# Optimization experiments

Hardware: AMD Instinct MI355X
Metric: run time of the kernel (lower is better)

Reference implementation:

```python
import jax, jax.numpy as jnp
import numpy as np

D_MODEL = 96
D_STATE = 16
D_CONV = 3
EXPAND = 2
D_INNER = D_MODEL * EXPAND          # 192
DT_RANK = max(1, D_MODEL // 16)     # 6
N_DIRS = 4
LN_EPS = 1e-5


def setup_inputs() -> dict:
    key = jax.random.key(0)
    ks = jax.random.split(key, 10)
    B, H, W = 2, 64, 64
    x = jax.random.normal(ks[0], (B, D_MODEL, H, W), dtype=jnp.float32)
    in_proj_w = jax.random.normal(ks[1], (2 * D_INNER, D_MODEL), dtype=jnp.float32) * 0.02
    conv_w = jax.random.normal(ks[2], (D_INNER, 1, D_CONV, D_CONV), dtype=jnp.float32) * 0.1
    conv_b = jnp.zeros((D_INNER,), dtype=jnp.float32)
    proj_dim = DT_RANK + 2 * D_STATE
    x_proj_weight = jax.random.normal(ks[3], (N_DIRS, D_INNER, proj_dim), dtype=jnp.float32) * 0.02
    dt_proj_weight = jax.random.normal(ks[4], (N_DIRS, D_INNER, DT_RANK), dtype=jnp.float32) * 0.02
    dt_proj_bias = jax.random.uniform(ks[5], (N_DIRS, D_INNER), dtype=jnp.float32) * 0.1
    A_log = jnp.log(jnp.broadcast_to(jnp.arange(1, D_STATE + 1, dtype=jnp.float32), (D_INNER, D_STATE)))
    D_skip = jnp.ones((D_INNER,), dtype=jnp.float32)
    ln_gamma = jnp.ones((D_INNER,), dtype=jnp.float32)
    ln_beta = jnp.zeros((D_INNER,), dtype=jnp.float32)
    out_proj_w = jax.random.normal(ks[6], (D_MODEL, D_INNER), dtype=jnp.float32) * 0.02
    return {
        "x": x, "in_proj_w": in_proj_w, "conv_w": conv_w, "conv_b": conv_b,
        "x_proj_weight": x_proj_weight, "dt_proj_weight": dt_proj_weight,
        "dt_proj_bias": dt_proj_bias, "A_log": A_log, "D_skip": D_skip,
        "ln_gamma": ln_gamma, "ln_beta": ln_beta, "out_proj_w": out_proj_w,
    }


def _ss2d_forward(x, in_proj_w, conv_w, conv_b, x_proj_weight, dt_proj_weight,
                  dt_proj_bias, A_log, D_skip, ln_gamma, ln_beta, out_proj_w):
    B, D, H, W = x.shape
    E, N, R = D_INNER, D_STATE, DT_RANK
    L = H * W
    # in_proj
    x_flat = x.reshape(B, D, L).transpose(0, 2, 1)              # b l d
    xz = x_flat @ in_proj_w.T                                    # b l 2e
    xb, z = xz[..., :E], xz[..., E:]
    # depthwise conv + SiLU
    xb = xb.transpose(0, 2, 1).reshape(B, E, H, W)
    xb = jax.lax.conv_general_dilated(
        xb, conv_w, window_strides=(1, 1), padding="SAME",
        feature_group_count=E, dimension_numbers=("NCHW", "OIHW", "NCHW"))
    xb = xb + conv_b[None, :, None, None]
    xb = jax.nn.silu(xb)
    # 4-directional cross-scan sequences
    x_rm = xb.reshape(B, E, L)
    x_cm = xb.transpose(0, 1, 3, 2).reshape(B, E, L)
    xs = jnp.stack([x_rm, x_rm[..., ::-1], x_cm, x_cm[..., ::-1]], axis=0)  # k b e l
    # per-direction projections
    x_for = xs.transpose(0, 1, 3, 2)                             # k b l e
    x_dbl = jnp.einsum("kble,ker->kblr", x_for, x_proj_weight)
    dt_low, Bs, Cs = x_dbl[..., :R], x_dbl[..., R:R + N], x_dbl[..., R + N:]
    dts = jnp.einsum("kblr,ker->kble", dt_low, dt_proj_weight) + dt_proj_bias[:, None, None, :]
    dt = jax.nn.softplus(dts)                                    # k b l e
    A = -jnp.exp(A_log)                                          # e n
    # batched selective scan over (k*b)
    KB = N_DIRS * B
    u = xs.reshape(KB, E, L)
    dt_ = dt.transpose(0, 1, 3, 2).reshape(KB, E, L)
    B_t = Bs.reshape(KB, L, N)
    C_t = Cs.reshape(KB, L, N)
    deltaA = jnp.exp(dt_[..., None] * A[None, :, None, :])       # kb e l n
    deltaBx = (dt_ * u)[..., None] * B_t[:, None, :, :]          # kb e l n

    def comb(c1, c2):
        a1, b1 = c1
        a2, b2 = c2
        return (a2 * a1, a2 * b1 + b2)

    _, h = jax.lax.associative_scan(comb, (deltaA, deltaBx), axis=2)  # kb e l n
    y = jnp.einsum("beln,bln->bel", h, C_t) + u * D_skip[None, :, None]
    ys = y.reshape(N_DIRS, B, E, L)
    y0, y1, y2, y3 = ys[0], ys[1][..., ::-1], ys[2], ys[3][..., ::-1]
    y_row = (y0 + y1).reshape(B, E, H, W)
    y_col = (y2 + y3).reshape(B, E, W, H).transpose(0, 1, 3, 2)
    yo = (y_row + y_col).reshape(B, E, L).transpose(0, 2, 1)     # b l e
    # LayerNorm over e
    mu = jnp.mean(yo, axis=-1, keepdims=True)
    var = jnp.mean((yo - mu) ** 2, axis=-1, keepdims=True)
    yo = (yo - mu) * jax.lax.rsqrt(var + LN_EPS) * ln_gamma + ln_beta
    yo = yo * jax.nn.silu(z)
    out = yo @ out_proj_w.T                                      # b l d
    return out.transpose(0, 2, 1).reshape(B, D, H, W)


def reference(x, in_proj_w, conv_w, conv_b, x_proj_weight, dt_proj_weight,
              dt_proj_bias, A_log, D_skip, ln_gamma, ln_beta, out_proj_w):
    return _ss2d_forward(x, in_proj_w, conv_w, conv_b, x_proj_weight,
                         dt_proj_weight, dt_proj_bias, A_log, D_skip,
                         ln_gamma, ln_beta, out_proj_w)
```

## Files before the change

kernel.cpp:

```cpp
#include <hip/hip_runtime.h>

#define LL 4096
#define HH 64
#define WWD 64
#define DM 96
#define EE 192
#define NN 16
#define RR 6
#define KBB 8
#define BB 2
#define CH 128
#define CLEN 32
#define SID (KBB * EE * NN)

__global__ __launch_bounds__(256) void k_inproj(const float* __restrict__ x,
                                                const float* __restrict__ W,
                                                float* __restrict__ xbuf,
                                                float* __restrict__ zbuf) {
    __shared__ float As[96][64];
    __shared__ float Ws[96][64];
    int bm = blockIdx.x;
    int bn = blockIdx.y;
    int l0 = bm * 64;
    int b  = l0 >> 12;
    int lb = l0 & (LL - 1);
    int j0 = bn * 64;
    int t  = threadIdx.x;

    for (int i = t; i < 96 * 64; i += 256) {
        int d = i >> 6, ml = i & 63;
        As[d][ml] = x[((size_t)b * 96 + d) * LL + lb + ml];
    }
    for (int i = t; i < 96 * 64; i += 256) {
        int jn = i / 96, d = i - jn * 96;
        Ws[d][jn] = W[(size_t)(j0 + jn) * 96 + d];
    }
    __syncthreads();

    int tx = t & 15, ty = t >> 4;
    float acc[4][4] = {};
    for (int d = 0; d < 96; d++) {
        float a[4], bbv[4];
        for (int i = 0; i < 4; i++) a[i] = As[d][ty * 4 + i];
        for (int j = 0; j < 4; j++) bbv[j] = Ws[d][tx * 4 + j];
        for (int i = 0; i < 4; i++)
            for (int j = 0; j < 4; j++) acc[i][j] = fmaf(a[i], bbv[j], acc[i][j]);
    }
    for (int i = 0; i < 4; i++) {
        int l = lb + ty * 4 + i;
        for (int j = 0; j < 4; j++) {
            int jj = j0 + tx * 4 + j;
            if (jj < EE)
                xbuf[((size_t)b * EE + jj) * LL + l] = acc[i][j];
            else
                zbuf[((size_t)b * LL + l) * EE + (jj - EE)] = acc[i][j];
        }
    }
}

__global__ __launch_bounds__(256) void k_conv(const float* __restrict__ xbuf,
                                              const float* __restrict__ cw,
                                              const float* __restrict__ cb,
                                              float* __restrict__ xconv) {
    int i = blockIdx.x * 256 + threadIdx.x;
    int pos = i & (LL - 1);
    int be  = i >> 12;
    int e   = be % EE;
    int h = pos >> 6, w = pos & 63;
    const float* src = xbuf + (size_t)be * LL;
    const float* wgt = cw + e * 9;
    float acc = cb[e];
    #pragma unroll
    for (int dh = -1; dh <= 1; dh++) {
        int hh = h + dh;
        if (hh < 0 || hh >= HH) continue;
        #pragma unroll
        for (int dw = -1; dw <= 1; dw++) {
            int w2 = w + dw;
            if (w2 < 0 || w2 >= WWD) continue;
            acc = fmaf(src[hh * WWD + w2], wgt[(dh + 1) * 3 + (dw + 1)], acc);
        }
    }
    xconv[i] = acc / (1.f + __expf(-acc));
}

__device__ __forceinline__ int seq_of_spatial(int k, int idx) {
    if (k == 0) return idx;
    if (k == 1) return LL - 1 - idx;
    int p = ((idx & 63) << 6) | (idx >> 6);
    if (k == 2) return p;
    return LL - 1 - p;
}

__device__ __forceinline__ int spatial_of_seq(int k, int l) {
    int lp = (k & 1) ? (LL - 1 - l) : l;
    return (k >= 2) ? (((lp & 63) << 6) | (lp >> 6)) : lp;
}

__global__ __launch_bounds__(256) void k_proj(const float* __restrict__ xconv,
                                              const float* __restrict__ xpw,
                                              const float* __restrict__ dtw,
                                              const float* __restrict__ dtb,
                                              float* __restrict__ dtbuf,
                                              float* __restrict__ Bbuf,
                                              float* __restrict__ Cbuf,
                                              float* __restrict__ xconv_t) {
    __shared__ float X[EE][65];
    __shared__ float PR[64][40];
    int kb = blockIdx.y;
    int k = kb >> 1, b = kb & 1;
    int t0 = blockIdx.x * 64;
    int t = threadIdx.x;

    for (int i = t; i < EE * 64; i += 256) {
        int e = i >> 6, p = i & 63;
        X[e][p] = xconv[((size_t)b * EE + e) * LL + t0 + p];
    }
    __syncthreads();
    if (kb < 2) {
        for (int i = t; i < 64 * EE; i += 256) {
            int p = i / EE, e = i - p * EE;
            xconv_t[((size_t)b * LL + t0 + p) * EE + e] = X[e][p];
        }
    }
    {
        int pos = t & 63;
        int obase = t >> 6;
        for (int oo = 0; oo < 40; oo += 4) {
            int out = oo + obase;
            if (out < 38) {
                float s = 0.f;
                const float* wp = xpw + (size_t)k * EE * 38 + out;
                for (int e = 0; e < EE; e++) s = fmaf(X[e][pos], wp[(size_t)e * 38], s);
                PR[pos][out] = s;
            }
        }
    }
    __syncthreads();
    for (int i = t; i < 64 * EE; i += 256) {
        int pos = i / EE, e = i - pos * EE;
        float s = dtb[k * EE + e];
        const float* wr = dtw + ((size_t)k * EE + e) * RR;
        #pragma unroll
        for (int r = 0; r < RR; r++) s = fmaf(PR[pos][r], wr[r], s);
        float sp = (s > 20.f) ? s : log1pf(__expf(s));
        int j = seq_of_spatial(k, t0 + pos);
        dtbuf[((size_t)kb * LL + j) * EE + e] = sp;
    }
    for (int i = t; i < 64 * 32; i += 256) {
        int pos = i >> 5, c = i & 31;
        int j = seq_of_spatial(k, t0 + pos);
        float v = PR[pos][6 + c];
        if (c < 16) Bbuf[((size_t)kb * LL + j) * NN + c] = v;
        else        Cbuf[((size_t)kb * LL + j) * NN + (c - 16)] = v;
    }
}

__global__ __launch_bounds__(192) void k_scan1(const float* __restrict__ xconv_t,
                                               const float* __restrict__ dtbuf,
                                               const float* __restrict__ Bbuf,
                                               const float* __restrict__ A_log,
                                               float* __restrict__ Ap,
                                               float* __restrict__ He) {
    __shared__ __align__(16) float sB[CLEN][NN];
    int c  = blockIdx.x;
    int kb = blockIdx.y;
    int k = kb >> 1, b = kb & 1;
    int e = threadIdx.x;
    int l0 = c * CLEN;

    for (int i = e; i < CLEN * NN; i += 192)
        ((float*)sB)[i] = Bbuf[((size_t)kb * LL + l0) * NN + i];

    float An[NN], h[NN], pa[NN];
    #pragma unroll
    for (int q = 0; q < 4; q++) {
        float4 al = *(const float4*)&A_log[e * NN + q * 4];
        An[q*4+0] = -__expf(al.x); An[q*4+1] = -__expf(al.y);
        An[q*4+2] = -__expf(al.z); An[q*4+3] = -__expf(al.w);
    }
    #pragma unroll
    for (int n = 0; n < NN; n++) { h[n] = 0.f; pa[n] = 1.f; }
    __syncthreads();

    const float* dtp = dtbuf + ((size_t)kb * LL + l0) * EE + e;
    const float* ub  = xconv_t + (size_t)b * LL * EE + e;

    #pragma unroll 2
    for (int i = 0; i < CLEN; i++) {
        int l = l0 + i;
        int idx = spatial_of_seq(k, l);
        float dtv = dtp[(size_t)i * EE];
        float u   = ub[(size_t)idx * EE];
        float Bv[NN];
        #pragma unroll
        for (int q = 0; q < 4; q++)
            *(float4*)&Bv[q*4] = ((const float4*)&sB[i][0])[q];
        float dtu = dtv * u;
        #pragma unroll
        for (int n = 0; n < NN; n++) {
            float a = __expf(dtv * An[n]);
            h[n] = fmaf(a, h[n], dtu * Bv[n]);
            pa[n] *= a;
        }
    }
    size_t sid = (size_t)c * SID + kb * (EE * NN) + e * NN;
    #pragma unroll
    for (int q = 0; q < 4; q++) {
        *(float4*)&Ap[sid + q*4] = make_float4(pa[q*4], pa[q*4+1], pa[q*4+2], pa[q*4+3]);
        *(float4*)&He[sid + q*4] = make_float4(h[q*4], h[q*4+1], h[q*4+2], h[q*4+3]);
    }
}

__global__ __launch_bounds__(256) void k_carry(float* __restrict__ ApHi,
                                               const float* __restrict__ He) {
    int sid = blockIdx.x * 256 + threadIdx.x;
    float h = 0.f;
    #pragma unroll 8
    for (int c = 0; c < CH; c++) {
        size_t ix = (size_t)c * SID + sid;
        float a  = ApHi[ix];
        float he = He[ix];
        ApHi[ix] = h;
        h = fmaf(a, h, he);
    }
}

__global__ __launch_bounds__(192) void k_scan2(const float* __restrict__ xconv_t,
                                               const float* __restrict__ dtbuf,
                                               const float* __restrict__ Bbuf,
                                               const float* __restrict__ Cbuf,
                                               const float* __restrict__ A_log,
                                               const float* __restrict__ Dskip,
                                               const float* __restrict__ Hi,
                                               float* __restrict__ yo) {
    __shared__ __align__(16) float sB[CLEN][NN];
    __shared__ __align__(16) float sC[CLEN][NN];
    int c  = blockIdx.x;
    int kb = blockIdx.y;
    int k = kb >> 1, b = kb & 1;
    int e = threadIdx.x;
    int l0 = c * CLEN;

    for (int i = e; i < CLEN * NN; i += 192) {
        ((float*)sB)[i] = Bbuf[((size_t)kb * LL + l0) * NN + i];
        ((float*)sC)[i] = Cbuf[((size_t)kb * LL + l0) * NN + i];
    }

    float An[NN], h[NN];
    #pragma unroll
    for (int q = 0; q < 4; q++) {
        float4 al = *(const float4*)&A_log[e * NN + q * 4];
        An[q*4+0] = -__expf(al.x); An[q*4+1] = -__expf(al.y);
        An[q*4+2] = -__expf(al.z); An[q*4+3] = -__expf(al.w);
    }
    size_t sid = (size_t)c * SID + kb * (EE * NN) + e * NN;
    #pragma unroll
    for (int q = 0; q < 4; q++) {
        float4 hv = *(const float4*)&Hi[sid + q*4];
        h[q*4+0] = hv.x; h[q*4+1] = hv.y; h[q*4+2] = hv.z; h[q*4+3] = hv.w;
    }
    float Dv = Dskip[e];
    __syncthreads();

    const float* dtp = dtbuf + ((size_t)kb * LL + l0) * EE + e;
    const float* ub  = xconv_t + (size_t)b * LL * EE + e;
    float* yob       = yo + (size_t)b * LL * EE + e;

    #pragma unroll 2
    for (int i = 0; i < CLEN; i++) {
        int l = l0 + i;
        int idx = spatial_of_seq(k, l);
        float dtv = dtp[(size_t)i * EE];
        float u   = ub[(size_t)idx * EE];
        float Bv[NN], Cv[NN];
        #pragma unroll
        for (int q = 0; q < 4; q++) {
            *(float4*)&Bv[q*4] = ((const float4*)&sB[i][0])[q];
            *(float4*)&Cv[q*4] = ((const float4*)&sC[i][0])[q];
        }
        float dtu = dtv * u;
        float y = u * Dv;
        #pragma unroll
        for (int n = 0; n < NN; n++) {
            float a = __expf(dtv * An[n]);
            h[n] = fmaf(a, h[n], dtu * Bv[n]);
            y = fmaf(h[n], Cv[n], y);
        }
        atomicAdd(&yob[(size_t)idx * EE], y);
    }
}

__global__ __launch_bounds__(256) void k_out(const float* __restrict__ yo,
                                             const float* __restrict__ zb,
                                             const float* __restrict__ gamma,
                                             const float* __restrict__ beta,
                                             const float* __restrict__ W2,
                                             float* __restrict__ out) {
    __shared__ float sbuf[32][193];
    int b  = blockIdx.x >> 7;
    int l0 = (blockIdx.x & 127) * 32;
    int t  = threadIdx.x;
    int wv = t >> 6, lane = t & 63;

    for (int li = 0; li < 32; li += 4) {
        int l = l0 + li + wv;
        const float* yrow = yo + ((size_t)b * LL + l) * EE;
        const float* zrow = zb + ((size_t)b * LL + l) * EE;
        float v[3], zv[3];
        float s = 0.f;
        #pragma unroll
        for (int j = 0; j < 3; j++) {
            v[j] = yrow[lane + 64 * j];
            zv[j] = zrow[lane + 64 * j];
            s += v[j];
        }
        for (int m = 1; m < 64; m <<= 1) s += __shfl_xor(s, m);
        float mu = s * (1.f / EE);
        float q = 0.f;
        #pragma unroll
        for (int j = 0; j < 3; j++) { float d = v[j] - mu; q = fmaf(d, d, q); }
        for (int m = 1; m < 64; m <<= 1) q += __shfl_xor(q, m);
        float rs = rsqrtf(q * (1.f / EE) + 1e-5f);
        #pragma unroll
        for (int j = 0; j < 3; j++) {
            int e = lane + 64 * j;
            float yn = (v[j] - mu) * rs * gamma[e] + beta[e];
            float zz = zv[j];
            float sil = zz / (1.f + __expf(-zz));
            sbuf[li + wv][e] = yn * sil;
        }
    }
    __syncthreads();
    for (int o = t; o < DM * 32; o += 256) {
        int d = o >> 5, c = o & 31;
        const float* wr = W2 + (size_t)d * EE;
        float acc = 0.f;
        for (int e = 0; e < EE; e++) acc = fmaf(sbuf[c][e], wr[e], acc);
        out[((size_t)b * DM + d) * LL + l0 + c] = acc;
    }
}

extern "C" void kernel_launch(void* const* d_in, const int* in_sizes, int n_in,
                              void* d_out, int out_size, void* d_ws, size_t ws_size,
                              hipStream_t stream) {
    const float* x      = (const float*)d_in[0];
    const float* in_w   = (const float*)d_in[1];
    const float* conv_w = (const float*)d_in[2];
    const float* conv_b = (const float*)d_in[3];
    const float* xpw    = (const float*)d_in[4];
    const float* dtw    = (const float*)d_in[5];
    const float* dtbias = (const float*)d_in[6];
    const float* A_log  = (const float*)d_in[7];
    const float* Dsk    = (const float*)d_in[8];
    const float* gamma  = (const float*)d_in[9];
    const float* beta   = (const float*)d_in[10];
    const float* W2     = (const float*)d_in[11];
    float* out = (float*)d_out;

    float* ws      = (float*)d_ws;
    float* xbuf    = ws;
    float* zbuf    = xbuf    + (size_t)BB * EE * LL;
    float* xconv   = zbuf    + (size_t)BB * LL * EE;
    float* xconv_t = xconv   + (size_t)BB * EE * LL;
    float* dtbuf   = xconv_t + (size_t)BB * LL * EE;
    float* Bbuf    = dtbuf   + (size_t)KBB * LL * EE;
    float* Cbuf    = Bbuf    + (size_t)KBB * LL * NN;
    float* yo      = Cbuf    + (size_t)KBB * LL * NN;
    float* ApHi    = yo      + (size_t)BB * LL * EE;
    float* He      = ApHi    + (size_t)CH * SID;

    hipMemsetAsync(yo, 0, (size_t)BB * LL * EE * sizeof(float), stream);

    k_inproj<<<dim3(128, 6), 256, 0, stream>>>(x, in_w, xbuf, zbuf);
    k_conv<<<(BB * EE * LL) / 256, 256, 0, stream>>>(xbuf, conv_w, conv_b, xconv);
    k_proj<<<dim3(64, 8), 256, 0, stream>>>(xconv, xpw, dtw, dtbias, dtbuf, Bbuf, Cbuf, xconv_t);
    k_scan1<<<dim3(CH, KBB), 192, 0, stream>>>(xconv_t, dtbuf, Bbuf, A_log, ApHi, He);
    k_carry<<<SID / 256, 256, 0, stream>>>(ApHi, He);
    k_scan2<<<dim3(CH, KBB), 192, 0, stream>>>(xconv_t, dtbuf, Bbuf, Cbuf, A_log, Dsk, ApHi, yo);
    k_out<<<BB * (LL / 32), 256, 0, stream>>>(yo, zbuf, gamma, beta, W2, out);
}
```

Before: 290.0 us.

## Fuse conv transpose output and merge four direction projections into one tiled GEMM

The depthwise conv kernel now also writes the transposed (b,l,e) copy through a shared-memory tile, removing that job from the projection kernel. The projection kernel is restructured so one block computes all four directions' x_proj outputs for 32 positions as a register-tiled GEMM with staged weights, reading xconv once instead of four times. The cost is a different block count, more shared memory per block, and redundant dt/B/C scatter loops per block.

```diff
diff --git a/kernel.cpp b/kernel.cpp
--- a/kernel.cpp
+++ b/kernel.cpp
@@ -61,27 +61,44 @@
 __global__ __launch_bounds__(256) void k_conv(const float* __restrict__ xbuf,
                                               const float* __restrict__ cw,
                                               const float* __restrict__ cb,
-                                              float* __restrict__ xconv) {
-    int i = blockIdx.x * 256 + threadIdx.x;
-    int pos = i & (LL - 1);
-    int be  = i >> 12;
-    int e   = be % EE;
+                                              float* __restrict__ xconv,
+                                              float* __restrict__ xconv_t) {
+    __shared__ float T[32][33];
+    int l0 = blockIdx.x * 32;
+    int e0 = blockIdx.y * 32;
+    int b  = blockIdx.z;
+    int t  = threadIdx.x;
+    int tp = t & 31, teo = t >> 5;
+
+    int pos = l0 + tp;
     int h = pos >> 6, w = pos & 63;
-    const float* src = xbuf + (size_t)be * LL;
-    const float* wgt = cw + e * 9;
-    float acc = cb[e];
-    #pragma unroll
-    for (int dh = -1; dh <= 1; dh++) {
-        int hh = h + dh;
-        if (hh < 0 || hh >= HH) continue;
-        #pragma unroll
-        for (int dw = -1; dw <= 1; dw++) {
-            int w2 = w + dw;
-            if (w2 < 0 || w2 >= WWD) continue;
-            acc = fmaf(src[hh * WWD + w2], wgt[(dh + 1) * 3 + (dw + 1)], acc);
-        }
-    }
-    xconv[i] = acc / (1.f + __expf(-acc));
+    #pragma unroll
+    for (int j = 0; j < 4; j++) {
+        int ee = j * 8 + teo;
+        int e = e0 + ee;
+        const float* src = xbuf + ((size_t)b * EE + e) * LL;
+        const float* wgt = cw + e * 9;
+        float acc = cb[e];
+        #pragma unroll
+        for (int dh = -1; dh <= 1; dh++) {
+            int hh = h + dh;
+            if (hh < 0 || hh >= HH) continue;
+            #pragma unroll
+            for (int dw = -1; dw <= 1; dw++) {
+                int w2 = w + dw;
+                if (w2 < 0 || w2 >= WWD) continue;
+                acc = fmaf(src[hh * WWD + w2], wgt[(dh + 1) * 3 + (dw + 1)], acc);
+            }
+        }
+        float v = acc / (1.f + __expf(-acc));
+        xconv[((size_t)b * EE + e) * LL + pos] = v;
+        T[ee][tp] = v;
+    }
+    __syncthreads();
+    for (int i = t; i < 32 * 32; i += 256) {
+        int p = i >> 5, ee = i & 31;
+        xconv_t[((size_t)b * LL + l0 + p) * EE + e0 + ee] = T[ee][p];
+    }
 }
 
 __device__ __forceinline__ int seq_of_spatial(int k, int idx) {
@@ -103,56 +120,88 @@
                                               const float* __restrict__ dtb,
                                               float* __restrict__ dtbuf,
                                               float* __restrict__ Bbuf,
-                                              float* __restrict__ Cbuf,
-                                              float* __restrict__ xconv_t) {
-    __shared__ float X[EE][65];
-    __shared__ float PR[64][40];
-    int kb = blockIdx.y;
-    int k = kb >> 1, b = kb & 1;
-    int t0 = blockIdx.x * 64;
-    int t = threadIdx.x;
-
-    for (int i = t; i < EE * 64; i += 256) {
-        int e = i >> 6, p = i & 63;
-        X[e][p] = xconv[((size_t)b * EE + e) * LL + t0 + p];
-    }
-    __syncthreads();
-    if (kb < 2) {
-        for (int i = t; i < 64 * EE; i += 256) {
-            int p = i / EE, e = i - p * EE;
-            xconv_t[((size_t)b * LL + t0 + p) * EE + e] = X[e][p];
-        }
-    }
-    {
-        int pos = t & 63;
-        int obase = t >> 6;
-        for (int oo = 0; oo < 40; oo += 4) {
-            int out = oo + obase;
-            if (out < 38) {
-                float s = 0.f;
-                const float* wp = xpw + (size_t)k * EE * 38 + out;
-                for (int e = 0; e < EE; e++) s = fmaf(X[e][pos], wp[(size_t)e * 38], s);
-                PR[pos][out] = s;
+                                              float* __restrict__ Cbuf) {
+    __shared__ float Ws[32][161];
+    __shared__ float PR[4][32][8];
+    __shared__ float BC[4][32][33];
+    int l0 = blockIdx.x * 32;
+    int b  = blockIdx.y;
+    int t  = threadIdx.x;
+    int pg = t >> 5;
+    int oc = t & 31;
+
+    float acc[4][5] = {};
+
+    for (int ep = 0; ep < 6; ep++) {
+        int e0 = ep * 32;
+        __syncthreads();
+        for (int i = t; i < 4 * 32 * 38; i += 256) {
+            int k = i / 1216;
+            int rem = i - k * 1216;
+            int ee = rem / 38, r = rem - ee * 38;
+            Ws[ee][k * 38 + r] = xpw[((size_t)k * EE + e0 + ee) * 38 + r];
+        }
+        for (int i = t; i < 32 * 9; i += 256) {
+            int ee = i / 9;
+            Ws[ee][152 + i % 9] = 0.f;
+        }
+        __syncthreads();
+        #pragma unroll 8
+        for (int ee = 0; ee < 32; ee++) {
+            int e = e0 + ee;
+            float4 xv = *(const float4*)&xconv[((size_t)b * EE + e) * LL + l0 + 4 * pg];
+            float wv[5];
+            #pragma unroll
+            for (int j = 0; j < 5; j++) wv[j] = Ws[ee][oc + 32 * j];
+            #pragma unroll
+            for (int j = 0; j < 5; j++) {
+                acc[0][j] = fmaf(xv.x, wv[j], acc[0][j]);
+                acc[1][j] = fmaf(xv.y, wv[j], acc[1][j]);
+                acc[2][j] = fmaf(xv.z, wv[j], acc[2][j]);
+                acc[3][j] = fmaf(xv.w, wv[j], acc[3][j]);
             }
         }
     }
-    __syncthreads();
-    for (int i = t; i < 64 * EE; i += 256) {
-        int pos = i / EE, e = i - pos * EE;
-        float s = dtb[k * EE + e];
-        const float* wr = dtw + ((size_t)k * EE + e) * RR;
-        #pragma unroll
-        for (int r = 0; r < RR; r++) s = fmaf(PR[pos][r], wr[r], s);
-        float sp = (s > 20.f) ? s : log1pf(__expf(s));
-        int j = seq_of_spatial(k, t0 + pos);
-        dtbuf[((size_t)kb * LL + j) * EE + e] = sp;
-    }
-    for (int i = t; i < 64 * 32; i += 256) {
-        int pos = i >> 5, c = i & 31;
-        int j = seq_of_spatial(k, t0 + pos);
-        float v = PR[pos][6 + c];
+
+    #pragma unroll
+    for (int j = 0; j < 5; j++) {
+        int col = oc + 32 * j;
+        if (col < 152) {
+            int k = (col >= 114) ? 3 : (col >= 76) ? 2 : (col >= 38) ? 1 : 0;
+            int r = col - k * 38;
+            #pragma unroll
+            for (int ii = 0; ii < 4; ii++) {
+                int pos = 4 * pg + ii;
+                if (r < 6) PR[k][pos][r] = acc[ii][j];
+                else       BC[k][pos][r - 6] = acc[ii][j];
+            }
+        }
+    }
+    __syncthreads();
+
+    for (int i = t; i < 4 * 32 * 32; i += 256) {
+        int kk = i >> 10;
+        int pos = (i >> 5) & 31;
+        int c = i & 31;
+        int j = seq_of_spatial(kk, l0 + pos);
+        float v = BC[kk][pos][c];
+        int kb = kk * 2 + b;
         if (c < 16) Bbuf[((size_t)kb * LL + j) * NN + c] = v;
         else        Cbuf[((size_t)kb * LL + j) * NN + (c - 16)] = v;
+    }
+
+    for (int i = t; i < 4 * 32 * EE; i += 256) {
+        int kp = i / EE;
+        int e = i - kp * EE;
+        int kk = kp >> 5, pos = kp & 31;
+        float s = dtb[kk * EE + e];
+        const float* wr = dtw + ((size_t)kk * EE + e) * RR;
+        #pragma unroll
+        for (int r = 0; r < RR; r++) s = fmaf(PR[kk][pos][r], wr[r], s);
+        float sp = (s > 20.f) ? s : log1pf(__expf(s));
+        int j = seq_of_spatial(kk, l0 + pos);
+        int kb = kk * 2 + b;
+        dtbuf[((size_t)kb * LL + j) * EE + e] = sp;
     }
 }
 
@@ -373,8 +422,8 @@
     hipMemsetAsync(yo, 0, (size_t)BB * LL * EE * sizeof(float), stream);
 
     k_inproj<<<dim3(128, 6), 256, 0, stream>>>(x, in_w, xbuf, zbuf);
-    k_conv<<<(BB * EE * LL) / 256, 256, 0, stream>>>(xbuf, conv_w, conv_b, xconv);
-    k_proj<<<dim3(64, 8), 256, 0, stream>>>(xconv, xpw, dtw, dtbias, dtbuf, Bbuf, Cbuf, xconv_t);
+    k_conv<<<dim3(128, 6, 2), 256, 0, stream>>>(xbuf, conv_w, conv_b, xconv, xconv_t);
+    k_proj<<<dim3(128, 2), 256, 0, stream>>>(xconv, xpw, dtw, dtbias, dtbuf, Bbuf, Cbuf);
     k_scan1<<<dim3(CH, KBB), 192, 0, stream>>>(xconv_t, dtbuf, Bbuf, A_log, ApHi, He);
     k_carry<<<SID / 256, 256, 0, stream>>>(ApHi, He);
     k_scan2<<<dim3(CH, KBB), 192, 0, stream>>>(xconv_t, dtbuf, Bbuf, Cbuf, A_log, Dsk, ApHi, yo);
```

Result: slower. 316.5 us (+9.1%).
